# Kernel optimization log

Measured on AMD Instinct MI355X. Metric: run time of the kernel, lower is better.

The kernel has to match this reference:

```python
import jax, jax.numpy as jnp
import numpy as np
from jax import lax

N, K, F = 512, 512, 96
DM = 256   # hidden_dim == d_model
DS = 256   # d_state (must equal d_model for the original code to run)
L = 2      # num_layers
EPS = 1e-5


def layer_norm(x, g, b):
    mu = jnp.mean(x, axis=-1, keepdims=True)
    var = jnp.var(x, axis=-1, keepdims=True)
    return (x - mu) * jax.lax.rsqrt(var + EPS) * g + b


def setup_inputs() -> dict:
    key = jax.random.key(0)
    ks = jax.random.split(key, 20)
    n = lambda k, shape, s=0.02: jax.random.normal(k, shape, dtype=jnp.float32) * s
    inp = {
        "x": jax.random.normal(ks[0], (N, K, F), dtype=jnp.float32),
        # input_proj
        "in_w": n(ks[1], (DM, F), 0.05), "in_b": jnp.zeros((DM,), jnp.float32),
        "in_ln_g": jnp.ones((DM,), jnp.float32), "in_ln_b": jnp.zeros((DM,), jnp.float32),
        # per-layer Mamba params, stacked on leading L axis
        "ln_g": jnp.ones((L, DM), jnp.float32), "ln_b": jnp.zeros((L, DM), jnp.float32),
        "gate_w": n(ks[2], (L, DM, DM), 0.05), "gate_b": jnp.zeros((L, DM), jnp.float32),
        "sp_w": n(ks[3], (L, DS, DM), 0.05), "sp_b": jnp.zeros((L, DS), jnp.float32),
        "op_w": n(ks[4], (L, DM, DM), 0.05), "op_b": jnp.zeros((L, DM), jnp.float32),
        "A_log": n(ks[5], (L, DM, DS), 0.02),
        "D": jnp.ones((L, DM), jnp.float32),
        # output_proj
        "out_w": n(ks[6], (DM, DM), 0.05), "out_b": jnp.zeros((DM,), jnp.float32),
        "out_ln_g": jnp.ones((DM,), jnp.float32), "out_ln_b": jnp.zeros((DM,), jnp.float32),
    }
    return inp


def _ssm_scan(state0, decay, s):
    # state_t = decay * state_{t-1} + s_t ; s: [N, K, DS]
    def step(st, s_t):
        st = st * decay + s_t
        return st, st
    state, states = lax.scan(step, state0, jnp.swapaxes(s, 0, 1))
    return state, jnp.swapaxes(states, 0, 1)  # [N, K, DS]


def reference(x, in_w, in_b, in_ln_g, in_ln_b, ln_g, ln_b, gate_w, gate_b,
              sp_w, sp_b, op_w, op_b, A_log, D, out_w, out_b, out_ln_g, out_ln_b):
    # input_proj: Linear -> LayerNorm -> GELU
    h = jnp.einsum('nkf,df->nkd', x, in_w) + in_b
    h = jax.nn.gelu(layer_norm(h, in_ln_g, in_ln_b), approximate=False)

    state = jnp.zeros((x.shape[0], DS), dtype=h.dtype)
    for l in range(L):
        res = h
        z = layer_norm(h, ln_g[l], ln_b[l])
        xg = jax.nn.silu(jnp.einsum('nkd,ed->nke', z, gate_w[l]) + gate_b[l])
        s = jnp.einsum('nkd,sd->nks', xg, sp_w[l]) + sp_b[l]          # state_proj
        decay = jnp.exp(-jnp.mean(jnp.exp(A_log[l]), axis=-1))         # exp(mean(A)), A=-exp(A_log)
        state, states = _ssm_scan(state, decay, s)
        y = jnp.einsum('nks,sd->nkd', states, sp_w[l]) + D[l] * xg     # matmul(state, W_sp) + D*u
        h = jnp.einsum('nkd,ed->nke', y, op_w[l]) + op_b[l] + res      # out_proj + residual

    pooled = h[:, -1, :]                                               # pooling='last'
    out = jnp.einsum('nd,ed->ne', pooled, out_w) + out_b
    out = jax.nn.gelu(layer_norm(out, out_ln_g, out_ln_b), approximate=False)
    return out
```

## Files before the change

kernel.cpp:

```cpp
#include <hip/hip_runtime.h>
#include <hip/hip_bf16.h>


typedef __attribute__((ext_vector_type(8))) __bf16 bf16x8;
typedef __attribute__((ext_vector_type(8))) short short8;
typedef __attribute__((ext_vector_type(4))) float f32x4;
typedef __attribute__((ext_vector_type(4))) unsigned u32x4;

#define NSEQ 512
#define KSEQ 512
#define FIN 96
#define DMODEL 256
#define MTOT (NSEQ*KSEQ)

__device__ __forceinline__ unsigned short f2bf(float f){
  union { float f; unsigned u; } v; v.f = f;
  unsigned r = (v.u + 0x7FFFu + ((v.u >> 16) & 1u)) >> 16;
  return (unsigned short)r;
}
__device__ __forceinline__ float bf2f(unsigned short b){
  union { unsigned u; float f; } v; v.u = ((unsigned)b) << 16; return v.f;
}
__device__ __forceinline__ unsigned pk_bf16(float lo, float hi){
  unsigned r;
  asm("v_cvt_pk_bf16_f32 %0, %1, %2" : "=v"(r) : "v"(lo), "v"(hi));
  return r;
}
__device__ __forceinline__ float gelu_f(float x){
  return 0.5f * x * (1.0f + erff(x * 0.70710678118654752440f));
}
__device__ __forceinline__ float silu_f(float x){
  return x / (1.0f + __expf(-x));
}
__device__ __forceinline__ void barx(){
  asm volatile("s_waitcnt lgkmcnt(0)" ::: "memory");
  __builtin_amdgcn_s_barrier();
}
__device__ __forceinline__ unsigned swzA(int row, int kbyte){
  return ((unsigned)(row*512 + kbyte)) ^ (unsigned)((row & 7) << 4);
}
__device__ __forceinline__ unsigned swzB(int n, int kbyte){
  return ((unsigned)(n*128 + kbyte)) ^ (unsigned)((n & 7) << 4);
}

__device__ __forceinline__ void gemm_w8(const unsigned short* __restrict__ wb,
                                        const char* As, f32x4 (&acc)[4][2],
                                        int lane, int c0)
{
  const int lr  = lane & 15;
  const int lk8 = (lane >> 4) * 8;
  const unsigned short* bp = wb + (size_t)(c0 + lr)*256 + lk8;
  bf16x8 bb[4][2];
  #pragma unroll
  for(int p = 0; p < 4; ++p)
    #pragma unroll
    for(int fc = 0; fc < 2; ++fc)
      bb[p][fc] = *(const bf16x8*)(bp + fc*4096 + p*32);
  #pragma unroll
  for(int kc = 0; kc < 8; ++kc){
    bf16x8 af[4];
    #pragma unroll
    for(int fr = 0; fr < 4; ++fr)
      af[fr] = *(const bf16x8*)(As + swzA(fr*16 + lr, kc*64 + lk8*2));
    #pragma unroll
    for(int fr = 0; fr < 4; ++fr)
      #pragma unroll
      for(int fc = 0; fc < 2; ++fc)
        acc[fr][fc] = __builtin_amdgcn_mfma_f32_16x16x32_bf16(af[fr], bb[kc&3][fc], acc[fr][fc], 0, 0, 0);
    if(kc < 4){
      #pragma unroll
      for(int fc = 0; fc < 2; ++fc)
        bb[kc&3][fc] = *(const bf16x8*)(bp + fc*4096 + (kc+4)*32);
    }
  }
}

__device__ __forceinline__ void zero_acc2(f32x4 (&acc)[4][2]){
  #pragma unroll
  for(int a=0;a<4;++a)
    #pragma unroll
    for(int b=0;b<2;++b)
      acc[a][b] = (f32x4){0.f,0.f,0.f,0.f};
}
__device__ __forceinline__ void zero_acc(f32x4 (&acc)[4][4]){
  #pragma unroll
  for(int a=0;a<4;++a)
    #pragma unroll
    for(int b=0;b<4;++b)
      acc[a][b] = (f32x4){0.f,0.f,0.f,0.f};
}

template<int KCH>
__device__ __forceinline__ void gemm_64x256(const unsigned short* __restrict__ wb,
                                            char* As, char* Bs,
                                            f32x4 (&acc)[4][4], int tid)
{
  const int lane = tid & 63;
  const int c0   = (tid >> 6) * 64;
  const int lr   = lane & 15;
  const int lk16 = (lane >> 4) * 16;
  #pragma unroll
  for(int kc = 0; kc < KCH; ++kc){
    __syncthreads();
    {
      const unsigned short* src = wb + (size_t)tid * (KCH*64) + kc*64;
      #pragma unroll
      for(int i = 0; i < 8; ++i){
        short8 v = *(const short8*)(src + i*8);
        *(short8*)(Bs + swzB(tid, i*16)) = v;
      }
    }
    __syncthreads();
    #pragma unroll
    for(int t2 = 0; t2 < 2; ++t2){
      bf16x8 af[4], bfr[4];
      #pragma unroll
      for(int fr = 0; fr < 4; ++fr)
        af[fr] = *(const bf16x8*)(As + swzA(fr*16 + lr, kc*128 + t2*64 + lk16));
      #pragma unroll
      for(int fc = 0; fc < 4; ++fc)
        bfr[fc] = *(const bf16x8*)(Bs + swzB(c0 + fc*16 + lr, t2*64 + lk16));
      #pragma unroll
      for(int fr = 0; fr < 4; ++fr)
        #pragma unroll
        for(int fc = 0; fc < 4; ++fc)
          acc[fr][fc] = __builtin_amdgcn_mfma_f32_16x16x32_bf16(af[fr], bfr[fc], acc[fr][fc], 0, 0, 0);
    }
  }
}

__global__ void k_cvt(const float* __restrict__ s, unsigned short* __restrict__ d, int n){
  int i = blockIdx.x*256 + threadIdx.x;
  if(i < n) d[i] = f2bf(s[i]);
}
__global__ void k_cvt_inw(const float* __restrict__ w, unsigned short* __restrict__ d){
  int i = blockIdx.x*256 + threadIdx.x;
  int n = i >> 7, f = i & 127;
  d[i] = (f < 96) ? f2bf(w[n*96 + f]) : (unsigned short)0;
}
__global__ void k_spT(const float* __restrict__ spw, unsigned short* __restrict__ d){
  int l = blockIdx.y;
  int i = blockIdx.x*256 + threadIdx.x;
  int dd = i >> 8, ss = i & 255;
  d[l*65536 + i] = f2bf(spw[l*65536 + ss*256 + dd]);
}
__global__ void k_decay(const float* __restrict__ A_log, float* __restrict__ decay){
  __shared__ float red[4];
  const int b = blockIdx.x;
  const int tid = threadIdx.x;
  float v = expf(A_log[(size_t)b*256 + tid]);
  #pragma unroll
  for(int o = 32; o >= 1; o >>= 1) v += __shfl_xor(v, o);
  if((tid & 63) == 0) red[tid >> 6] = v;
  __syncthreads();
  if(tid == 0){
    float s = red[0] + red[1] + red[2] + red[3];
    decay[b] = expf(-s * (1.f/256.f));
  }
}

__global__ __launch_bounds__(256) void k_in_proj(
    const float* __restrict__ x_g,
    const unsigned short* __restrict__ in_wb,
    const float* __restrict__ in_b,
    const float* __restrict__ ln_gv, const float* __restrict__ ln_bv,
    unsigned short* __restrict__ h_g)
{
  __shared__ char smem[65536];
  char* As = smem; char* Bs = smem + 32768;
  const int tid = threadIdx.x;
  const int m0 = blockIdx.x * 64;
  const int lane = tid & 63, c0w = (tid>>6)*64, lr = lane & 15, rb = (lane>>4)*4;
  {
    const int r = tid >> 2, cq = tid & 3;
    const float* src = x_g + (size_t)(m0 + r)*FIN + cq*24;
    unsigned short tmp[24] __attribute__((aligned(16)));
    #pragma unroll
    for(int i = 0; i < 6; ++i){
      float4 v = *(const float4*)(src + i*4);
      tmp[4*i]=f2bf(v.x); tmp[4*i+1]=f2bf(v.y); tmp[4*i+2]=f2bf(v.z); tmp[4*i+3]=f2bf(v.w);
    }
    #pragma unroll
    for(int i = 0; i < 3; ++i)
      *(short8*)(As + swzA(r, cq*48 + i*16)) = *(const short8*)(tmp + i*8);
    if(cq == 3){
      short8 z8 = {0,0,0,0,0,0,0,0};
      #pragma unroll
      for(int i = 0; i < 4; ++i)
        *(short8*)(As + swzA(r, 192 + i*16)) = z8;
    }
  }
  f32x4 acc[4][4]; zero_acc(acc);
  gemm_64x256<2>(in_wb, As, Bs, acc, tid);
  __syncthreads();
  #pragma unroll
  for(int fc = 0; fc < 4; ++fc){
    const int col = c0w + fc*16 + lr;
    const float bb = in_b[col];
    #pragma unroll
    for(int fr = 0; fr < 4; ++fr)
      #pragma unroll
      for(int rg = 0; rg < 4; ++rg){
        const int row = fr*16 + rb + rg;
        *(float*)(smem + (((unsigned)(row*1024 + col*4)) ^ ((row&7)<<4))) = acc[fr][fc][rg] + bb;
      }
  }
  __syncthreads();
  {
    const int r = tid >> 2, c0 = (tid & 3) * 64;
    float vals[64]; float sm = 0.f, sq = 0.f;
    #pragma unroll
    for(int i = 0; i < 16; ++i){
      float4 v = *(const float4*)(smem + (((unsigned)(r*1024 + (c0 + i*4)*4)) ^ ((r&7)<<4)));
      vals[4*i]=v.x; vals[4*i+1]=v.y; vals[4*i+2]=v.z; vals[4*i+3]=v.w;
    }
    #pragma unroll
    for(int i = 0; i < 64; ++i){ sm += vals[i]; sq += vals[i]*vals[i]; }
    sm += __shfl_xor(sm, 1); sm += __shfl_xor(sm, 2);
    sq += __shfl_xor(sq, 1); sq += __shfl_xor(sq, 2);
    const float mu = sm * (1.f/256.f);
    const float rstd = rsqrtf(sq * (1.f/256.f) - mu*mu + 1e-5f);
    unsigned short* dst = h_g + (size_t)(m0 + r)*DMODEL + c0;
    #pragma unroll
    for(int i = 0; i < 8; ++i){
      float g[8];
      #pragma unroll
      for(int j = 0; j < 8; ++j){
        const int c = c0 + i*8 + j;
        g[j] = gelu_f((vals[i*8+j]-mu)*rstd*ln_gv[c] + ln_bv[c]);
      }
      u32x4 o;
      o[0] = pk_bf16(g[0],g[1]); o[1] = pk_bf16(g[2],g[3]);
      o[2] = pk_bf16(g[4],g[5]); o[3] = pk_bf16(g[6],g[7]);
      *(u32x4*)(dst + i*8) = o;
    }
  }
}

__global__ __launch_bounds__(512,2) void k_layers(
    unsigned short* __restrict__ h_g,
    const unsigned short* __restrict__ gate_w0,
    const unsigned short* __restrict__ sp_w0,
    const unsigned short* __restrict__ spT_w0,
    const unsigned short* __restrict__ op_w0,
    const float* __restrict__ ln_g0, const float* __restrict__ ln_b0,
    const float* __restrict__ gate_b0, const float* __restrict__ sp_b0,
    const float* __restrict__ decay0, const float* __restrict__ D0,
    const float* __restrict__ op_b0)
{
  __shared__ char As[32768];
  __shared__ char Ss[32768];
  const int tid = threadIdx.x;
  const int n = blockIdx.x;
  const int lane = tid & 63;
  const int c0w = (tid >> 6) * 32;
  const int lr = lane & 15, rb = (lane>>4)*4;
  const int rA = tid >> 3, cAh = (tid & 7) * 32;
  float st = 0.f;

  #pragma unroll 1
  for(int l = 0; l < 2; ++l){
    const unsigned short* gw  = gate_w0 + l*65536;
    const unsigned short* spw = sp_w0   + l*65536;
    const unsigned short* spT = spT_w0  + l*65536;
    const unsigned short* opw = op_w0   + l*65536;
    const float* lg  = ln_g0   + l*256;
    const float* lb  = ln_b0   + l*256;
    const float* gb_ = gate_b0 + l*256;
    const float* sb_ = sp_b0   + l*256;
    const float* Dv_ = D0      + l*256;
    const float* ob_ = op_b0   + l*256;
    const float dc = decay0[l*256 + (tid & 255)];

    #pragma unroll 1
    for(int kb = 0; kb < 8; ++kb){
      const int m0 = n*KSEQ + kb*64;
      {
        const unsigned short* src = h_g + (size_t)(m0 + rA)*DMODEL + cAh;
        short8 hv[4];
        #pragma unroll
        for(int i = 0; i < 4; ++i) hv[i] = *(const short8*)(src + i*8);
        float sm = 0.f, sq = 0.f;
        #pragma unroll
        for(int i = 0; i < 4; ++i)
          #pragma unroll
          for(int j = 0; j < 8; ++j){
            float v = bf2f((unsigned short)hv[i][j]); sm += v; sq += v*v;
          }
        sm += __shfl_xor(sm, 1); sm += __shfl_xor(sm, 2); sm += __shfl_xor(sm, 4);
        sq += __shfl_xor(sq, 1); sq += __shfl_xor(sq, 2); sq += __shfl_xor(sq, 4);
        const float mu = sm * (1.f/256.f);
        const float rstd = rsqrtf(sq * (1.f/256.f) - mu*mu + 1e-5f);
        #pragma unroll
        for(int i = 0; i < 4; ++i){
          float z[8];
          #pragma unroll
          for(int j = 0; j < 8; ++j){
            const int c = cAh + i*8 + j;
            z[j] = (bf2f((unsigned short)hv[i][j])-mu)*rstd*lg[c] + lb[c];
          }
          u32x4 zz;
          zz[0] = pk_bf16(z[0],z[1]); zz[1] = pk_bf16(z[2],z[3]);
          zz[2] = pk_bf16(z[4],z[5]); zz[3] = pk_bf16(z[6],z[7]);
          *(u32x4*)(As + swzA(rA, cAh*2 + i*16)) = zz;
        }
      }
      barx();
      f32x4 acc[4][2]; zero_acc2(acc);
      gemm_w8(gw, As, acc, lane, c0w);
      #pragma unroll
      for(int fc = 0; fc < 2; ++fc){
        const int col = c0w + fc*16 + lr;
        const float gb = gb_[col];
        #pragma unroll
        for(int fr = 0; fr < 4; ++fr){
          const int row = fr*16 + rb;
          float v0 = silu_f(acc[fr][fc][0] + gb), v1 = silu_f(acc[fr][fc][1] + gb);
          float v2 = silu_f(acc[fr][fc][2] + gb), v3 = silu_f(acc[fr][fc][3] + gb);
          unsigned p0 = pk_bf16(v0, v1), p1 = pk_bf16(v2, v3);
          *(unsigned short*)(Ss + swzA(row+0, col*2)) = (unsigned short)p0;
          *(unsigned short*)(Ss + swzA(row+1, col*2)) = (unsigned short)(p0 >> 16);
          *(unsigned short*)(Ss + swzA(row+2, col*2)) = (unsigned short)p1;
          *(unsigned short*)(Ss + swzA(row+3, col*2)) = (unsigned short)(p1 >> 16);
        }
      }
      barx();
      zero_acc2(acc);
      gemm_w8(spw, Ss, acc, lane, c0w);
      #pragma unroll
      for(int fc = 0; fc < 2; ++fc){
        const int col = c0w + fc*16 + lr;
        const float sb = sb_[col];
        #pragma unroll
        for(int fr = 0; fr < 4; ++fr){
          const int row = fr*16 + rb;
          unsigned p0 = pk_bf16(acc[fr][fc][0] + sb, acc[fr][fc][1] + sb);
          unsigned p1 = pk_bf16(acc[fr][fc][2] + sb, acc[fr][fc][3] + sb);
          *(unsigned short*)(As + swzA(row+0, col*2)) = (unsigned short)p0;
          *(unsigned short*)(As + swzA(row+1, col*2)) = (unsigned short)(p0 >> 16);
          *(unsigned short*)(As + swzA(row+2, col*2)) = (unsigned short)p1;
          *(unsigned short*)(As + swzA(row+3, col*2)) = (unsigned short)(p1 >> 16);
        }
      }
      barx();
      if(tid < 256){
        #pragma unroll
        for(int c4 = 0; c4 < 4; ++c4){
          const int base = c4*16;
          float v[16];
          #pragma unroll
          for(int j = 0; j < 16; ++j)
            v[j] = bf2f(*(const unsigned short*)(As + swzA(base+j, tid*2)));
          #pragma unroll
          for(int j = 0; j < 16; ++j){ st = st*dc + v[j]; v[j] = st; }
          #pragma unroll
          for(int j = 0; j < 8; ++j){
            unsigned p = pk_bf16(v[2*j], v[2*j+1]);
            *(unsigned short*)(As + swzA(base+2*j,   tid*2)) = (unsigned short)p;
            *(unsigned short*)(As + swzA(base+2*j+1, tid*2)) = (unsigned short)(p >> 16);
          }
        }
      }
      barx();
      zero_acc2(acc);
      gemm_w8(spT, As, acc, lane, c0w);
      #pragma unroll
      for(int fc = 0; fc < 2; ++fc){
        const int col = c0w + fc*16 + lr;
        const float Dv = Dv_[col];
        #pragma unroll
        for(int fr = 0; fr < 4; ++fr){
          const int row = fr*16 + rb;
          float y0 = acc[fr][fc][0] + Dv*bf2f(*(const unsigned short*)(Ss + swzA(row+0, col*2)));
          float y1 = acc[fr][fc][1] + Dv*bf2f(*(const unsigned short*)(Ss + swzA(row+1, col*2)));
          float y2 = acc[fr][fc][2] + Dv*bf2f(*(const unsigned short*)(Ss + swzA(row+2, col*2)));
          float y3 = acc[fr][fc][3] + Dv*bf2f(*(const unsigned short*)(Ss + swzA(row+3, col*2)));
          unsigned p0 = pk_bf16(y0, y1), p1 = pk_bf16(y2, y3);
          *(unsigned short*)(Ss + swzA(row+0, col*2)) = (unsigned short)p0;
          *(unsigned short*)(Ss + swzA(row+1, col*2)) = (unsigned short)(p0 >> 16);
          *(unsigned short*)(Ss + swzA(row+2, col*2)) = (unsigned short)p1;
          *(unsigned short*)(Ss + swzA(row+3, col*2)) = (unsigned short)(p1 >> 16);
        }
      }
      barx();
      zero_acc2(acc);
      gemm_w8(opw, Ss, acc, lane, c0w);
      #pragma unroll
      for(int fc = 0; fc < 2; ++fc){
        const int col = c0w + fc*16 + lr;
        const float ob = ob_[col];
        #pragma unroll
        for(int fr = 0; fr < 4; ++fr){
          const int row = fr*16 + rb;
          unsigned p0 = pk_bf16(acc[fr][fc][0] + ob, acc[fr][fc][1] + ob);
          unsigned p1 = pk_bf16(acc[fr][fc][2] + ob, acc[fr][fc][3] + ob);
          *(unsigned short*)(As + swzA(row+0, col*2)) = (unsigned short)p0;
          *(unsigned short*)(As + swzA(row+1, col*2)) = (unsigned short)(p0 >> 16);
          *(unsigned short*)(As + swzA(row+2, col*2)) = (unsigned short)p1;
          *(unsigned short*)(As + swzA(row+3, col*2)) = (unsigned short)(p1 >> 16);
        }
      }
      {
        char* hb = (char*)(h_g + (size_t)m0*DMODEL);
        const int cl = lane & 3;
        const int rbase = lane >> 2;
        #pragma unroll
        for(int p = 0; p < 4; ++p){
          const int row = p*16 + rbase;
          const unsigned gof = (unsigned)(row*512 + c0w*2 + cl*16);
          short8 a = *(const short8*)(As + swzA(row, c0w*2 + cl*16));
          short8 hv = *(const short8*)(hb + gof);
          u32x4 o;
          #pragma unroll
          for(int j = 0; j < 4; ++j){
            float s0 = bf2f((unsigned short)a[2*j])   + bf2f((unsigned short)hv[2*j]);
            float s1 = bf2f((unsigned short)a[2*j+1]) + bf2f((unsigned short)hv[2*j+1]);
            o[j] = pk_bf16(s0, s1);
          }
          *(u32x4*)(hb + gof) = o;
        }
      }
      barx();
    }
  }
}

__global__ __launch_bounds__(256) void k_out(
    const unsigned short* __restrict__ h_g,
    const unsigned short* __restrict__ out_wb,
    const float* __restrict__ out_bv,
    const float* __restrict__ ln_gv, const float* __restrict__ ln_bv,
    float* __restrict__ out_g)
{
  __shared__ char smem[65536];
  char* As = smem; char* Bs = smem + 32768;
  const int tid = threadIdx.x;
  const int r0 = blockIdx.x * 64;
  const int lane = tid & 63, c0w = (tid>>6)*64, lr = lane & 15, rb = (lane>>4)*4;
  {
    const int r = tid >> 2, c0 = (tid & 3) * 64;
    const unsigned short* src = h_g + ((size_t)(r0 + r)*KSEQ + (KSEQ-1))*DMODEL + c0;
    #pragma unroll
    for(int i = 0; i < 8; ++i){
      short8 v = *(const short8*)(src + i*8);
      *(short8*)(As + swzA(r, c0*2 + i*16)) = v;
    }
  }
  f32x4 acc[4][4]; zero_acc(acc);
  gemm_64x256<4>(out_wb, As, Bs, acc, tid);
  __syncthreads();
  #pragma unroll
  for(int fc = 0; fc < 4; ++fc){
    const int col = c0w + fc*16 + lr;
    const float bb = out_bv[col];
    #pragma unroll
    for(int fr = 0; fr < 4; ++fr)
      #pragma unroll
      for(int rg = 0; rg < 4; ++rg){
        const int row = fr*16 + rb + rg;
        *(float*)(smem + (((unsigned)(row*1024 + col*4)) ^ ((row&7)<<4))) = acc[fr][fc][rg] + bb;
      }
  }
  __syncthreads();
  {
    const int r = tid >> 2, c0 = (tid & 3) * 64;
    float vals[64]; float sm = 0.f, sq = 0.f;
    #pragma unroll
    for(int i = 0; i < 16; ++i){
      float4 v = *(const float4*)(smem + (((unsigned)(r*1024 + (c0 + i*4)*4)) ^ ((r&7)<<4)));
      vals[4*i]=v.x; vals[4*i+1]=v.y; vals[4*i+2]=v.z; vals[4*i+3]=v.w;
    }
    #pragma unroll
    for(int i = 0; i < 64; ++i){ sm += vals[i]; sq += vals[i]*vals[i]; }
    sm += __shfl_xor(sm, 1); sm += __shfl_xor(sm, 2);
    sq += __shfl_xor(sq, 1); sq += __shfl_xor(sq, 2);
    const float mu = sm * (1.f/256.f);
    const float rstd = rsqrtf(sq * (1.f/256.f) - mu*mu + 1e-5f);
    float* dst = out_g + (size_t)(r0 + r)*DMODEL + c0;
    #pragma unroll
    for(int i = 0; i < 16; ++i){
      float4 o;
      o.x = gelu_f((vals[4*i+0]-mu)*rstd*ln_gv[c0+i*4+0] + ln_bv[c0+i*4+0]);
      o.y = gelu_f((vals[4*i+1]-mu)*rstd*ln_gv[c0+i*4+1] + ln_bv[c0+i*4+1]);
      o.z = gelu_f((vals[4*i+2]-mu)*rstd*ln_gv[c0+i*4+2] + ln_bv[c0+i*4+2]);
      o.w = gelu_f((vals[4*i+3]-mu)*rstd*ln_gv[c0+i*4+3] + ln_bv[c0+i*4+3]);
      *(float4*)(dst + i*4) = o;
    }
  }
}

extern "C" void kernel_launch(void* const* d_in, const int* in_sizes, int n_in,
                              void* d_out, int out_size, void* d_ws, size_t ws_size,
                              hipStream_t stream) {
  (void)in_sizes; (void)n_in; (void)out_size; (void)ws_size;
  const float* x        = (const float*)d_in[0];
  const float* in_w     = (const float*)d_in[1];
  const float* in_b     = (const float*)d_in[2];
  const float* in_ln_g  = (const float*)d_in[3];
  const float* in_ln_b  = (const float*)d_in[4];
  const float* ln_g     = (const float*)d_in[5];
  const float* ln_b     = (const float*)d_in[6];
  const float* gate_w   = (const float*)d_in[7];
  const float* gate_b   = (const float*)d_in[8];
  const float* sp_w     = (const float*)d_in[9];
  const float* sp_b     = (const float*)d_in[10];
  const float* op_w     = (const float*)d_in[11];
  const float* op_b     = (const float*)d_in[12];
  const float* A_log    = (const float*)d_in[13];
  const float* Dp       = (const float*)d_in[14];
  const float* out_w    = (const float*)d_in[15];
  const float* out_b    = (const float*)d_in[16];
  const float* out_ln_g = (const float*)d_in[17];
  const float* out_ln_b = (const float*)d_in[18];

  char* ws = (char*)d_ws;
  unsigned short* h_g       = (unsigned short*)(ws + 0);
  float*          decay     = (float*)(ws + 134217728);
  unsigned short* wbase     = (unsigned short*)(ws + 134219776);
  unsigned short* in_wb  = wbase;
  unsigned short* gate_wb= in_wb  + 32768;
  unsigned short* sp_wb  = gate_wb+ 131072;
  unsigned short* sp_wTb = sp_wb  + 131072;
  unsigned short* op_wb  = sp_wTb + 131072;
  unsigned short* out_wb = op_wb  + 131072;

  k_cvt_inw<<<128, 256, 0, stream>>>(in_w, in_wb);
  k_cvt<<<512, 256, 0, stream>>>(gate_w, gate_wb, 131072);
  k_cvt<<<512, 256, 0, stream>>>(sp_w,   sp_wb,   131072);
  k_cvt<<<512, 256, 0, stream>>>(op_w,   op_wb,   131072);
  k_cvt<<<256, 256, 0, stream>>>(out_w,  out_wb,  65536);
  k_spT<<<dim3(256,2), 256, 0, stream>>>(sp_w, sp_wTb);
  k_decay<<<512, 256, 0, stream>>>(A_log, decay);

  k_in_proj<<<MTOT/64, 256, 0, stream>>>(x, in_wb, in_b, in_ln_g, in_ln_b, h_g);
  k_layers<<<NSEQ, 512, 0, stream>>>(h_g, gate_wb, sp_wb, sp_wTb, op_wb,
      ln_g, ln_b, gate_b, sp_b, decay, Dp, op_b);
  k_out<<<NSEQ/64, 256, 0, stream>>>(h_g, out_wb, out_b, out_ln_g, out_ln_b, (float*)d_out);
}
```

Baseline: 1.100 ms.

## Software-pipeline sequence chunks with double-buffered LDS to overlap scan and GEMMs

Splits the per-chunk layer body into phase functions and double-buffers the A and S shared-memory tiles. The LayerNorm, gate GEMM and state-projection GEMM for the next 64-row chunk now run alongside the scan, y-GEMM and output-projection GEMM of the current chunk. This cuts block barriers per chunk from six to three and hides the serial scan behind independent MMA work. The cost is that shared memory per block doubles to 128 KB, which likely limits each CU to one resident 512-thread block instead of two.

```diff
diff --git a/kernel.cpp b/kernel.cpp
--- a/kernel.cpp
+++ b/kernel.cpp
@@ -32,10 +32,6 @@
 __device__ __forceinline__ float silu_f(float x){
   return x / (1.0f + __expf(-x));
 }
-__device__ __forceinline__ void barx(){
-  asm volatile("s_waitcnt lgkmcnt(0)" ::: "memory");
-  __builtin_amdgcn_s_barrier();
-}
 __device__ __forceinline__ unsigned swzA(int row, int kbyte){
   return ((unsigned)(row*512 + kbyte)) ^ (unsigned)((row & 7) << 4);
 }
@@ -88,6 +84,179 @@
     #pragma unroll
     for(int b=0;b<4;++b)
       acc[a][b] = (f32x4){0.f,0.f,0.f,0.f};
+}
+
+__device__ __forceinline__ void ph_ln(const unsigned short* __restrict__ h_g, int m0,
+    char* A, const float* __restrict__ lg, const float* __restrict__ lb,
+    int rA, int cAh)
+{
+  const unsigned short* src = h_g + (size_t)(m0 + rA)*DMODEL + cAh;
+  short8 hv[4];
+  #pragma unroll
+  for(int i = 0; i < 4; ++i) hv[i] = *(const short8*)(src + i*8);
+  float sm = 0.f, sq = 0.f;
+  #pragma unroll
+  for(int i = 0; i < 4; ++i)
+    #pragma unroll
+    for(int j = 0; j < 8; ++j){
+      float v = bf2f((unsigned short)hv[i][j]); sm += v; sq += v*v;
+    }
+  sm += __shfl_xor(sm, 1); sm += __shfl_xor(sm, 2); sm += __shfl_xor(sm, 4);
+  sq += __shfl_xor(sq, 1); sq += __shfl_xor(sq, 2); sq += __shfl_xor(sq, 4);
+  const float mu = sm * (1.f/256.f);
+  const float rstd = rsqrtf(sq * (1.f/256.f) - mu*mu + 1e-5f);
+  #pragma unroll
+  for(int i = 0; i < 4; ++i){
+    float z[8];
+    #pragma unroll
+    for(int j = 0; j < 8; ++j){
+      const int c = cAh + i*8 + j;
+      z[j] = (bf2f((unsigned short)hv[i][j])-mu)*rstd*lg[c] + lb[c];
+    }
+    u32x4 zz;
+    zz[0] = pk_bf16(z[0],z[1]); zz[1] = pk_bf16(z[2],z[3]);
+    zz[2] = pk_bf16(z[4],z[5]); zz[3] = pk_bf16(z[6],z[7]);
+    *(u32x4*)(A + swzA(rA, cAh*2 + i*16)) = zz;
+  }
+}
+
+__device__ __forceinline__ void ph_gate(const unsigned short* __restrict__ gw,
+    const char* A, char* S, const float* __restrict__ gb_,
+    int lane, int c0w, int lr, int rb)
+{
+  f32x4 acc[4][2]; zero_acc2(acc);
+  gemm_w8(gw, A, acc, lane, c0w);
+  #pragma unroll
+  for(int fc = 0; fc < 2; ++fc){
+    const int col = c0w + fc*16 + lr;
+    const float gb = gb_[col];
+    #pragma unroll
+    for(int fr = 0; fr < 4; ++fr){
+      const int row = fr*16 + rb;
+      float v0 = silu_f(acc[fr][fc][0] + gb), v1 = silu_f(acc[fr][fc][1] + gb);
+      float v2 = silu_f(acc[fr][fc][2] + gb), v3 = silu_f(acc[fr][fc][3] + gb);
+      unsigned p0 = pk_bf16(v0, v1), p1 = pk_bf16(v2, v3);
+      *(unsigned short*)(S + swzA(row+0, col*2)) = (unsigned short)p0;
+      *(unsigned short*)(S + swzA(row+1, col*2)) = (unsigned short)(p0 >> 16);
+      *(unsigned short*)(S + swzA(row+2, col*2)) = (unsigned short)p1;
+      *(unsigned short*)(S + swzA(row+3, col*2)) = (unsigned short)(p1 >> 16);
+    }
+  }
+}
+
+__device__ __forceinline__ void ph_sp(const unsigned short* __restrict__ spw,
+    const char* S, char* A, const float* __restrict__ sb_,
+    int lane, int c0w, int lr, int rb)
+{
+  f32x4 acc[4][2]; zero_acc2(acc);
+  gemm_w8(spw, S, acc, lane, c0w);
+  #pragma unroll
+  for(int fc = 0; fc < 2; ++fc){
+    const int col = c0w + fc*16 + lr;
+    const float sb = sb_[col];
+    #pragma unroll
+    for(int fr = 0; fr < 4; ++fr){
+      const int row = fr*16 + rb;
+      unsigned p0 = pk_bf16(acc[fr][fc][0] + sb, acc[fr][fc][1] + sb);
+      unsigned p1 = pk_bf16(acc[fr][fc][2] + sb, acc[fr][fc][3] + sb);
+      *(unsigned short*)(A + swzA(row+0, col*2)) = (unsigned short)p0;
+      *(unsigned short*)(A + swzA(row+1, col*2)) = (unsigned short)(p0 >> 16);
+      *(unsigned short*)(A + swzA(row+2, col*2)) = (unsigned short)p1;
+      *(unsigned short*)(A + swzA(row+3, col*2)) = (unsigned short)(p1 >> 16);
+    }
+  }
+}
+
+__device__ __forceinline__ void ph_scan(char* A, float& st, float dc, int tid)
+{
+  if(tid < 256){
+    #pragma unroll
+    for(int c4 = 0; c4 < 4; ++c4){
+      const int base = c4*16;
+      float v[16];
+      #pragma unroll
+      for(int j = 0; j < 16; ++j)
+        v[j] = bf2f(*(const unsigned short*)(A + swzA(base+j, tid*2)));
+      #pragma unroll
+      for(int j = 0; j < 16; ++j){ st = st*dc + v[j]; v[j] = st; }
+      #pragma unroll
+      for(int j = 0; j < 8; ++j){
+        unsigned p = pk_bf16(v[2*j], v[2*j+1]);
+        *(unsigned short*)(A + swzA(base+2*j,   tid*2)) = (unsigned short)p;
+        *(unsigned short*)(A + swzA(base+2*j+1, tid*2)) = (unsigned short)(p >> 16);
+      }
+    }
+  }
+}
+
+__device__ __forceinline__ void ph_spt_y(const unsigned short* __restrict__ spT,
+    const char* A, char* S, const float* __restrict__ Dv_,
+    int lane, int c0w, int lr, int rb)
+{
+  f32x4 acc[4][2]; zero_acc2(acc);
+  gemm_w8(spT, A, acc, lane, c0w);
+  #pragma unroll
+  for(int fc = 0; fc < 2; ++fc){
+    const int col = c0w + fc*16 + lr;
+    const float Dv = Dv_[col];
+    #pragma unroll
+    for(int fr = 0; fr < 4; ++fr){
+      const int row = fr*16 + rb;
+      float y0 = acc[fr][fc][0] + Dv*bf2f(*(const unsigned short*)(S + swzA(row+0, col*2)));
+      float y1 = acc[fr][fc][1] + Dv*bf2f(*(const unsigned short*)(S + swzA(row+1, col*2)));
+      float y2 = acc[fr][fc][2] + Dv*bf2f(*(const unsigned short*)(S + swzA(row+2, col*2)));
+      float y3 = acc[fr][fc][3] + Dv*bf2f(*(const unsigned short*)(S + swzA(row+3, col*2)));
+      unsigned p0 = pk_bf16(y0, y1), p1 = pk_bf16(y2, y3);
+      *(unsigned short*)(S + swzA(row+0, col*2)) = (unsigned short)p0;
+      *(unsigned short*)(S + swzA(row+1, col*2)) = (unsigned short)(p0 >> 16);
+      *(unsigned short*)(S + swzA(row+2, col*2)) = (unsigned short)p1;
+      *(unsigned short*)(S + swzA(row+3, col*2)) = (unsigned short)(p1 >> 16);
+    }
+  }
+}
+
+__device__ __forceinline__ void ph_op_rmw(const unsigned short* __restrict__ opw,
+    const char* S, char* A, const float* __restrict__ ob_,
+    unsigned short* __restrict__ h_g, int m0,
+    int lane, int c0w, int lr, int rb)
+{
+  f32x4 acc[4][2]; zero_acc2(acc);
+  gemm_w8(opw, S, acc, lane, c0w);
+  #pragma unroll
+  for(int fc = 0; fc < 2; ++fc){
+    const int col = c0w + fc*16 + lr;
+    const float ob = ob_[col];
+    #pragma unroll
+    for(int fr = 0; fr < 4; ++fr){
+      const int row = fr*16 + rb;
+      unsigned p0 = pk_bf16(acc[fr][fc][0] + ob, acc[fr][fc][1] + ob);
+      unsigned p1 = pk_bf16(acc[fr][fc][2] + ob, acc[fr][fc][3] + ob);
+      *(unsigned short*)(A + swzA(row+0, col*2)) = (unsigned short)p0;
+      *(unsigned short*)(A + swzA(row+1, col*2)) = (unsigned short)(p0 >> 16);
+      *(unsigned short*)(A + swzA(row+2, col*2)) = (unsigned short)p1;
+      *(unsigned short*)(A + swzA(row+3, col*2)) = (unsigned short)(p1 >> 16);
+    }
+  }
+  {
+    char* hb = (char*)(h_g + (size_t)m0*DMODEL);
+    const int cl = lane & 3;
+    const int rbase = lane >> 2;
+    #pragma unroll
+    for(int p = 0; p < 4; ++p){
+      const int row = p*16 + rbase;
+      const unsigned gof = (unsigned)(row*512 + c0w*2 + cl*16);
+      short8 a = *(const short8*)(A + swzA(row, c0w*2 + cl*16));
+      short8 hv = *(const short8*)(hb + gof);
+      u32x4 o;
+      #pragma unroll
+      for(int j = 0; j < 4; ++j){
+        float s0 = bf2f((unsigned short)a[2*j])   + bf2f((unsigned short)hv[2*j]);
+        float s1 = bf2f((unsigned short)a[2*j+1]) + bf2f((unsigned short)hv[2*j+1]);
+        o[j] = pk_bf16(s0, s1);
+      }
+      *(u32x4*)(hb + gof) = o;
+    }
+  }
 }
 
 template<int KCH>
@@ -248,8 +417,10 @@
     const float* __restrict__ decay0, const float* __restrict__ D0,
     const float* __restrict__ op_b0)
 {
-  __shared__ char As[32768];
-  __shared__ char Ss[32768];
+  __shared__ char As0[32768];
+  __shared__ char Ss0[32768];
+  __shared__ char As1[32768];
+  __shared__ char Ss1[32768];
   const int tid = threadIdx.x;
   const int n = blockIdx.x;
   const int lane = tid & 63;
@@ -271,156 +442,31 @@
     const float* Dv_ = D0      + l*256;
     const float* ob_ = op_b0   + l*256;
     const float dc = decay0[l*256 + (tid & 255)];
+    const int mL = n*KSEQ;
+
+    ph_ln(h_g, mL, As0, lg, lb, rA, cAh);
+    __syncthreads();
+    ph_gate(gw, As0, Ss0, gb_, lane, c0w, lr, rb);
+    __syncthreads();
+    ph_sp(spw, Ss0, As0, sb_, lane, c0w, lr, rb);
+    __syncthreads();
 
     #pragma unroll 1
     for(int kb = 0; kb < 8; ++kb){
-      const int m0 = n*KSEQ + kb*64;
-      {
-        const unsigned short* src = h_g + (size_t)(m0 + rA)*DMODEL + cAh;
-        short8 hv[4];
-        #pragma unroll
-        for(int i = 0; i < 4; ++i) hv[i] = *(const short8*)(src + i*8);
-        float sm = 0.f, sq = 0.f;
-        #pragma unroll
-        for(int i = 0; i < 4; ++i)
-          #pragma unroll
-          for(int j = 0; j < 8; ++j){
-            float v = bf2f((unsigned short)hv[i][j]); sm += v; sq += v*v;
-          }
-        sm += __shfl_xor(sm, 1); sm += __shfl_xor(sm, 2); sm += __shfl_xor(sm, 4);
-        sq += __shfl_xor(sq, 1); sq += __shfl_xor(sq, 2); sq += __shfl_xor(sq, 4);
-        const float mu = sm * (1.f/256.f);
-        const float rstd = rsqrtf(sq * (1.f/256.f) - mu*mu + 1e-5f);
-        #pragma unroll
-        for(int i = 0; i < 4; ++i){
-          float z[8];
-          #pragma unroll
-          for(int j = 0; j < 8; ++j){
-            const int c = cAh + i*8 + j;
-            z[j] = (bf2f((unsigned short)hv[i][j])-mu)*rstd*lg[c] + lb[c];
-          }
-          u32x4 zz;
-          zz[0] = pk_bf16(z[0],z[1]); zz[1] = pk_bf16(z[2],z[3]);
-          zz[2] = pk_bf16(z[4],z[5]); zz[3] = pk_bf16(z[6],z[7]);
-          *(u32x4*)(As + swzA(rA, cAh*2 + i*16)) = zz;
-        }
-      }
-      barx();
-      f32x4 acc[4][2]; zero_acc2(acc);
-      gemm_w8(gw, As, acc, lane, c0w);
-      #pragma unroll
-      for(int fc = 0; fc < 2; ++fc){
-        const int col = c0w + fc*16 + lr;
-        const float gb = gb_[col];
-        #pragma unroll
-        for(int fr = 0; fr < 4; ++fr){
-          const int row = fr*16 + rb;
-          float v0 = silu_f(acc[fr][fc][0] + gb), v1 = silu_f(acc[fr][fc][1] + gb);
-          float v2 = silu_f(acc[fr][fc][2] + gb), v3 = silu_f(acc[fr][fc][3] + gb);
-          unsigned p0 = pk_bf16(v0, v1), p1 = pk_bf16(v2, v3);
-          *(unsigned short*)(Ss + swzA(row+0, col*2)) = (unsigned short)p0;
-          *(unsigned short*)(Ss + swzA(row+1, col*2)) = (unsigned short)(p0 >> 16);
-          *(unsigned short*)(Ss + swzA(row+2, col*2)) = (unsigned short)p1;
-          *(unsigned short*)(Ss + swzA(row+3, col*2)) = (unsigned short)(p1 >> 16);
-        }
-      }
-      barx();
-      zero_acc2(acc);
-      gemm_w8(spw, Ss, acc, lane, c0w);
-      #pragma unroll
-      for(int fc = 0; fc < 2; ++fc){
-        const int col = c0w + fc*16 + lr;
-        const float sb = sb_[col];
-        #pragma unroll
-        for(int fr = 0; fr < 4; ++fr){
-          const int row = fr*16 + rb;
-          unsigned p0 = pk_bf16(acc[fr][fc][0] + sb, acc[fr][fc][1] + sb);
-          unsigned p1 = pk_bf16(acc[fr][fc][2] + sb, acc[fr][fc][3] + sb);
-          *(unsigned short*)(As + swzA(row+0, col*2)) = (unsigned short)p0;
-          *(unsigned short*)(As + swzA(row+1, col*2)) = (unsigned short)(p0 >> 16);
-          *(unsigned short*)(As + swzA(row+2, col*2)) = (unsigned short)p1;
-          *(unsigned short*)(As + swzA(row+3, col*2)) = (unsigned short)(p1 >> 16);
-        }
-      }
-      barx();
-      if(tid < 256){
-        #pragma unroll
-        for(int c4 = 0; c4 < 4; ++c4){
-          const int base = c4*16;
-          float v[16];
-          #pragma unroll
-          for(int j = 0; j < 16; ++j)
-            v[j] = bf2f(*(const unsigned short*)(As + swzA(base+j, tid*2)));
-          #pragma unroll
-          for(int j = 0; j < 16; ++j){ st = st*dc + v[j]; v[j] = st; }
-          #pragma unroll
-          for(int j = 0; j < 8; ++j){
-            unsigned p = pk_bf16(v[2*j], v[2*j+1]);
-            *(unsigned short*)(As + swzA(base+2*j,   tid*2)) = (unsigned short)p;
-            *(unsigned short*)(As + swzA(base+2*j+1, tid*2)) = (unsigned short)(p >> 16);
-          }
-        }
-      }
-      barx();
-      zero_acc2(acc);
-      gemm_w8(spT, As, acc, lane, c0w);
-      #pragma unroll
-      for(int fc = 0; fc < 2; ++fc){
-        const int col = c0w + fc*16 + lr;
-        const float Dv = Dv_[col];
-        #pragma unroll
-        for(int fr = 0; fr < 4; ++fr){
-          const int row = fr*16 + rb;
-          float y0 = acc[fr][fc][0] + Dv*bf2f(*(const unsigned short*)(Ss + swzA(row+0, col*2)));
-          float y1 = acc[fr][fc][1] + Dv*bf2f(*(const unsigned short*)(Ss + swzA(row+1, col*2)));
-          float y2 = acc[fr][fc][2] + Dv*bf2f(*(const unsigned short*)(Ss + swzA(row+2, col*2)));
-          float y3 = acc[fr][fc][3] + Dv*bf2f(*(const unsigned short*)(Ss + swzA(row+3, col*2)));
-          unsigned p0 = pk_bf16(y0, y1), p1 = pk_bf16(y2, y3);
-          *(unsigned short*)(Ss + swzA(row+0, col*2)) = (unsigned short)p0;
-          *(unsigned short*)(Ss + swzA(row+1, col*2)) = (unsigned short)(p0 >> 16);
-          *(unsigned short*)(Ss + swzA(row+2, col*2)) = (unsigned short)p1;
-          *(unsigned short*)(Ss + swzA(row+3, col*2)) = (unsigned short)(p1 >> 16);
-        }
-      }
-      barx();
-      zero_acc2(acc);
-      gemm_w8(opw, Ss, acc, lane, c0w);
-      #pragma unroll
-      for(int fc = 0; fc < 2; ++fc){
-        const int col = c0w + fc*16 + lr;
-        const float ob = ob_[col];
-        #pragma unroll
-        for(int fr = 0; fr < 4; ++fr){
-          const int row = fr*16 + rb;
-          unsigned p0 = pk_bf16(acc[fr][fc][0] + ob, acc[fr][fc][1] + ob);
-          unsigned p1 = pk_bf16(acc[fr][fc][2] + ob, acc[fr][fc][3] + ob);
-          *(unsigned short*)(As + swzA(row+0, col*2)) = (unsigned short)p0;
-          *(unsigned short*)(As + swzA(row+1, col*2)) = (unsigned short)(p0 >> 16);
-          *(unsigned short*)(As + swzA(row+2, col*2)) = (unsigned short)p1;
-          *(unsigned short*)(As + swzA(row+3, col*2)) = (unsigned short)(p1 >> 16);
-        }
-      }
-      {
-        char* hb = (char*)(h_g + (size_t)m0*DMODEL);
-        const int cl = lane & 3;
-        const int rbase = lane >> 2;
-        #pragma unroll
-        for(int p = 0; p < 4; ++p){
-          const int row = p*16 + rbase;
-          const unsigned gof = (unsigned)(row*512 + c0w*2 + cl*16);
-          short8 a = *(const short8*)(As + swzA(row, c0w*2 + cl*16));
-          short8 hv = *(const short8*)(hb + gof);
-          u32x4 o;
-          #pragma unroll
-          for(int j = 0; j < 4; ++j){
-            float s0 = bf2f((unsigned short)a[2*j])   + bf2f((unsigned short)hv[2*j]);
-            float s1 = bf2f((unsigned short)a[2*j+1]) + bf2f((unsigned short)hv[2*j+1]);
-            o[j] = pk_bf16(s0, s1);
-          }
-          *(u32x4*)(hb + gof) = o;
-        }
-      }
-      barx();
+      char* Ab = (kb & 1) ? As1 : As0;
+      char* Sb = (kb & 1) ? Ss1 : Ss0;
+      char* Af = (kb & 1) ? As0 : As1;
+      char* Sf = (kb & 1) ? Ss0 : Ss1;
+      const int m0 = mL + kb*64;
+      if(kb < 7) ph_ln(h_g, m0 + 64, Af, lg, lb, rA, cAh);
+      ph_scan(Ab, st, dc, tid);
+      __syncthreads();
+      ph_spt_y(spT, Ab, Sb, Dv_, lane, c0w, lr, rb);
+      if(kb < 7) ph_gate(gw, Af, Sf, gb_, lane, c0w, lr, rb);
+      __syncthreads();
+      ph_op_rmw(opw, Sb, Ab, ob_, h_g, m0, lane, c0w, lr, rb);
+      if(kb < 7) ph_sp(spw, Sf, Af, sb_, lane, c0w, lr, rb);
+      __syncthreads();
     }
   }
 }
```

Measured after the change: 1.032 ms. 6.2% less time.
